# Kernel optimization log

Hardware: AMD Instinct MI355X
Metric: run time of the kernel (lower is better)

## Reference

```python
import jax, jax.numpy as jnp
import numpy as np

E = 2_000_000
N = 50_000   # num nodes / agents (static for segment ops)
D = 32       # emb_dim
L = 2        # num_layers


def setup_inputs() -> dict:
    key = jax.random.key(0)
    ks = jax.random.split(key, 20)
    s = 0.1
    inp = {
        'edge_attr': jax.random.normal(ks[0], (E, 1), jnp.float32),
        'edge_index': jax.random.randint(ks[1], (2, E), 0, N, jnp.int32),
        'w_in': jax.random.normal(ks[2], (1, D)) * s,
        'b_in': jax.random.normal(ks[3], (D,)) * s,
        'tw1': jax.random.normal(ks[4], (L, D, D)) * s,
        'tb1': jax.random.normal(ks[5], (L, D)) * s,
        'tw2': jax.random.normal(ks[6], (L, D, D)) * s,
        'tb2': jax.random.normal(ks[7], (L, D)) * s,
        'uw1': jax.random.normal(ks[8], (L, 2 * D, D)) * s,
        'ub1': jax.random.normal(ks[9], (L, D)) * s,
        'uw2': jax.random.normal(ks[10], (L, D, D)) * s,
        'ub2': jax.random.normal(ks[11], (L, D)) * s,
        'hw1': jax.random.normal(ks[12], (2 * D, D)) * s,
        'hb1': jax.random.normal(ks[13], (D,)) * s,
        'hw2': jax.random.normal(ks[14], (D, D)) * s,
        'hb2': jax.random.normal(ks[15], (D,)) * s,
        'hw3': jax.random.normal(ks[16], (D, 1)) * s,
        'hb3': jax.random.normal(ks[17], (1,)) * s,
    }
    return inp


def reference(edge_attr, edge_index, w_in, b_in, tw1, tb1, tw2, tb2,
              uw1, ub1, uw2, ub2, hw1, hb1, hw2, hb2, hw3, hb3):
    lrelu = jax.nn.leaky_relu  # negative_slope=0.01, matches torch default
    idx = edge_index[0]  # [E] source node per edge

    h0 = edge_attr @ w_in + b_in      # [E, D]
    h = h0
    for l in range(L):
        # per-edge transform MLP
        t = lrelu(h @ tw1[l] + tb1[l]) @ tw2[l] + tb2[l]          # [E, D]
        # scatter_add over source node, then gather back
        s = jax.ops.segment_sum(t, idx, num_segments=N)            # [N, D]
        a = jnp.concatenate([h, s[idx]], axis=-1)                  # [E, 2D]
        h = lrelu(a @ uw1[l] + ub1[l]) @ uw2[l] + ub2[l]           # [E, D]

    hcat = jnp.concatenate([h0, h], axis=-1)                       # [E, 2D]
    v = lrelu(hcat @ hw1 + hb1)
    v = lrelu(v @ hw2 + hb2)
    values = (v @ hw3 + hb3)[:, 0]                                 # [E]

    # constraint == 'sum': scatter_softmax over edge_index[0], times 1.0
    m = jax.ops.segment_max(values, idx, num_segments=N)           # [N]
    e = jnp.exp(values - m[idx])
    d = jax.ops.segment_sum(e, idx, num_segments=N)                # [N]
    votes = (e / d[idx])[:, None] * 1.0                            # [E, 1]
    return votes
```

## Files before the change

### kernel.cpp

```cpp
#include <hip/hip_runtime.h>

#define NN 50000
#define DD 32
#define BLK 256

typedef float f32x4 __attribute__((ext_vector_type(4)));
typedef _Float16 f16x8 __attribute__((ext_vector_type(8)));
typedef __fp16 fp16x2 __attribute__((ext_vector_type(2)));

struct __align__(8) EdgeRec {
    float a;
    int src;
};

union H8 {
    f16x8 h;
    unsigned u[4];
    uint4 u4;
};

__device__ __forceinline__ float lrelu(float x) { return fmaxf(x, 0.01f * x); }

__device__ __forceinline__ f32x4 lrelu4(f32x4 v) {
    f32x4 r;
    r[0] = fmaxf(v[0], 0.01f * v[0]);
    r[1] = fmaxf(v[1], 0.01f * v[1]);
    r[2] = fmaxf(v[2], 0.01f * v[2]);
    r[3] = fmaxf(v[3], 0.01f * v[3]);
    return r;
}

__device__ __forceinline__ unsigned pkrtz(float a, float b) {
    union {
        fp16x2 h;
        unsigned u;
    } x;
    x.h = __builtin_amdgcn_cvt_pkrtz(a, b);
    return x.u;
}

__device__ __forceinline__ f32x4 ld4(const float* __restrict__ p) {
    return *(const f32x4*)p;
}

__device__ __forceinline__ void lds_copy(float* dst, const float* __restrict__ src, int n) {
    for (int i = threadIdx.x; i < n; i += blockDim.x) dst[i] = src[i];
}

__global__ __launch_bounds__(256) void k_hist(const int* __restrict__ ei, int* __restrict__ cnt,
                                              int nE) {
    int e = blockIdx.x * 256 + threadIdx.x;
    if (e < nE) atomicAdd(&cnt[ei[e]], 1);
}

__global__ __launch_bounds__(1024) void k_scan(int* __restrict__ cnt_cur, int* __restrict__ off,
                                               int nN) {
    __shared__ int part[1024];
    int t = threadIdx.x;
    const int CH = (nN + 1023) / 1024;
    int beg = t * CH, end = min(beg + CH, nN);
    int sum = 0;
    for (int i = beg; i < end; ++i) sum += cnt_cur[i];
    part[t] = sum;
    __syncthreads();
    for (int ofs = 1; ofs < 1024; ofs <<= 1) {
        int v = (t >= ofs) ? part[t - ofs] : 0;
        __syncthreads();
        part[t] += v;
        __syncthreads();
    }
    int run = (t == 0) ? 0 : part[t - 1];
    for (int i = beg; i < end; ++i) {
        int c = cnt_cur[i];
        off[i] = run;
        cnt_cur[i] = run;
        run += c;
    }
    if (t == 1023) off[nN] = part[1023];
}

__global__ __launch_bounds__(256) void k_fill(const int* __restrict__ ei,
                                              const float* __restrict__ ea, int* __restrict__ cur,
                                              EdgeRec* __restrict__ rec, int* __restrict__ inv,
                                              int nE) {
    int e = blockIdx.x * 256 + threadIdx.x;
    if (e >= nE) return;
    int src = ei[e];
    int pos = atomicAdd(&cur[src], 1);
    reinterpret_cast<int2*>(rec)[pos] = make_int2(__float_as_int(ea[e]), src);
    inv[e] = pos;
}

__global__ __launch_bounds__(256) void k_bstart(const int* __restrict__ offs,
                                                int* __restrict__ nstart, int nB, int nE) {
    int b = blockIdx.x * 256 + threadIdx.x;
    if (b > nB) return;
    int s = min(b * BLK, nE - 1);
    int lo = 0, hi = NN - 1;
    while (lo < hi) {
        int mid = (lo + hi + 1) >> 1;
        if (offs[mid] <= s) lo = mid;
        else hi = mid - 1;
    }
    nstart[b] = lo;
}

__global__ __launch_bounds__(192) void k_prep(const float* __restrict__ w_in,
                                              const float* __restrict__ b_in,
                                              const float* __restrict__ tw1,
                                              const float* __restrict__ tb1,
                                              const float* __restrict__ uw1,
                                              const float* __restrict__ ub1,
                                              const float* __restrict__ hw1,
                                              const float* __restrict__ hb1,
                                              float* __restrict__ pre) {
    int t = threadIdx.x;
    int which = t >> 5, f = t & 31;
    if (which >= 6) return;
    const float* W = (which < 2) ? tw1 : (which < 4) ? uw1 : hw1;
    const float* x = (which & 1) ? b_in : w_in;
    const float* badd = (which == 1) ? tb1 : (which == 3) ? ub1 : (which == 5) ? hb1 : nullptr;
    float s = badd ? badd[f] : 0.f;
    for (int k = 0; k < 32; ++k) s = fmaf(x[k], W[k * 32 + f], s);
    pre[which * 32 + f] = s;
}

__global__ __launch_bounds__(256) void k_prep2(
    const float* __restrict__ tw1, const float* __restrict__ tb1, const float* __restrict__ tw2,
    const float* __restrict__ tb2, const float* __restrict__ uw1, const float* __restrict__ ub1,
    const float* __restrict__ uw2, const float* __restrict__ ub2, const float* __restrict__ hw1,
    const float* __restrict__ hw2, const float* __restrict__ pre, float* __restrict__ fold,
    unsigned* __restrict__ fragu) {
    for (int e = threadIdx.x; e < 5 * 1024 + 5 * 32; e += 256) {
        if (e < 5120) {
            int m = e >> 10, r = e & 1023, i = r >> 5, j = r & 31;
            const float* A;
            const float* B;
            switch (m) {
                case 0: A = uw2;        B = uw1 + 2048; break;
                case 1: A = uw2;        B = tw1 + 1024; break;
                case 2: A = tw2;        B = uw1 + 1024; break;
                case 3: A = tw2 + 1024; B = uw1 + 3072; break;
                default: A = uw2 + 1024; B = hw1 + 1024; break;
            }
            float s = 0.f;
            for (int k = 0; k < 32; ++k) s = fmaf(A[i * 32 + k], B[k * 32 + j], s);
            fold[e] = s;
        } else {
            int r = e - 5120;
            int v = r >> 5, f = r & 31;
            const float* x;
            const float* B;
            float s;
            switch (v) {
                case 0: x = ub2;      B = tw1 + 1024; s = tb1[32 + f]; break;
                case 1: x = tb2;      B = uw1 + 1024; s = 0.f;         break;
                case 2: x = tb2 + 32; B = uw1 + 3072; s = 0.f;         break;
                case 3: x = ub2;      B = uw1 + 2048; s = ub1[32 + f]; break;
                default: x = ub2 + 32; B = hw1 + 1024; s = pre[160 + f]; break;
            }
            for (int k = 0; k < 32; ++k) s = fmaf(x[k], B[k * 32 + f], s);
            fold[e] = s;
        }
    }
    __syncthreads();
    for (int idx = threadIdx.x; idx < 2048; idx += 256) {
        int d = idx & 3;
        int l = (idx >> 2) & 63;
        int T = (idx >> 8) & 1;
        int m = idx >> 9;
        int row = 16 * T + (l & 15);
        int k0 = ((l >> 4) << 3) + 2 * d;
        const float* W = (m == 0) ? fold + 1024 : (m == 1) ? fold : (m == 2) ? fold + 4096 : hw2;
        int phi = (m == 3) ? row : (((row >> 2) & 3) * 8 + ((row >> 4) << 2) + (row & 3));
        union {
            _Float16 h[2];
            unsigned u;
        } P;
        P.h[0] = (_Float16)W[k0 * 32 + phi];
        P.h[1] = (_Float16)W[(k0 + 1) * 32 + phi];
        fragu[idx] = P.u;
    }
}

__global__ __launch_bounds__(256) void k_accum0f(const EdgeRec* __restrict__ rec,
                                                 const int* __restrict__ offs,
                                                 const int* __restrict__ nstart,
                                                 const float* __restrict__ pre,
                                                 float* __restrict__ M0, int nE) {
    __shared__ float zs[256 * 33];
    __shared__ int woff[260];
    __shared__ int sh2[2];
    int tid = threadIdx.x, b = blockIdx.x;
    int s0 = b * BLK, s1 = min(s0 + BLK, nE);
    if (tid == 0) {
        int nlo = nstart[b];
        sh2[0] = nlo;
        sh2[1] = nstart[b + 1] - nlo + 1;
    }
    __syncthreads();
    int nlo = sh2[0], nwin = sh2[1];
    for (int i = tid; i < nwin + 1; i += 256) woff[i] = offs[nlo + i];
    int s = s0 + tid;
    if (s < s1) {
        float a = rec[s].a;
#pragma unroll
        for (int f = 0; f < DD; ++f) zs[tid * 33 + f] = lrelu(fmaf(a, pre[f], pre[32 + f]));
    }
    __syncthreads();
    for (int t = tid; t < nwin * DD; t += 256) {
        int ln = t >> 5, f = t & 31;
        int lo = max(woff[ln], s0), hi = min(woff[ln + 1], s1);
        if (lo >= hi) continue;
        float sum = 0.f;
        for (int j = lo; j < hi; ++j) sum += zs[(j - s0) * 33 + f];
        int n = nlo + ln;
        bool interior = (woff[ln] >= s0) && (woff[ln + 1] <= s1);
        if (interior) M0[(size_t)n * DD + f] = sum;
        else atomicAdd(&M0[(size_t)n * DD + f], sum);
    }
}

__global__ __launch_bounds__(256) void k_gnode(const float* __restrict__ M,
                                               const float* __restrict__ W,
                                               const float* __restrict__ dv,
                                               const float* __restrict__ addv,
                                               const int* __restrict__ off, float* __restrict__ g) {
    __shared__ float LW[1088];
    lds_copy(LW, W, 1024);
    lds_copy(LW + 1024, dv, 32);
    lds_copy(LW + 1056, addv, 32);
    __syncthreads();
    int tid = blockIdx.x * 256 + threadIdx.x;
    int n = tid >> 5, f = tid & 31;
    if (n >= NN) return;
    float deg = (float)(off[n + 1] - off[n]);
    const float* srow = M + (size_t)n * DD;
    float acc = fmaf(deg, LW[1024 + f], LW[1056 + f]);
    for (int k = 0; k < 32; ++k) acc = fmaf(srow[k], LW[k * 32 + f], acc);
    g[(size_t)n * DD + f] = acc;
}

__global__ __launch_bounds__(256) void k_z1m(const EdgeRec* __restrict__ rec,
                                             const int* __restrict__ offs,
                                             const int* __restrict__ nstart,
                                             const float* __restrict__ pre,
                                             const float* __restrict__ fold,
                                             const unsigned* __restrict__ fragu,
                                             const float* __restrict__ g1, float* __restrict__ Z1,
                                             int nE) {
    __shared__ __align__(16) float zs[256 * 36];
    __shared__ int woff[260];
    __shared__ int sh2[2];
    int tid = threadIdx.x, b = blockIdx.x;
    int s0 = b * BLK, s1 = min(s0 + BLK, nE);
    if (tid == 0) {
        int nlo = nstart[b];
        sh2[0] = nlo;
        sh2[1] = nstart[b + 1] - nlo + 1;
    }
    __syncthreads();
    int nlo = sh2[0], nwin = sh2[1];
    for (int i = tid; i < nwin + 1; i += 256) woff[i] = offs[nlo + i];

    int l = tid & 63, g = l >> 4, e = l & 15, wv = tid >> 6;
    const uint4* fb = (const uint4*)fragu;
    H8 WB0, WB1;
    WB0.u4 = fb[0 + l];
    WB1.u4 = fb[64 + l];
    f32x4 cua = ld4(pre + 64 + 8 * g), cub = ld4(pre + 64 + 8 * g + 4);
    f32x4 vBa = ld4(fold + 5120 + 8 * g), vBb = ld4(fold + 5120 + 8 * g + 4);

    for (int c = 0; c < 4; ++c) {
        int ls = wv * 64 + c * 16 + e;
        int slot = s0 + ls;
        int sc = min(slot, nE - 1);
        EdgeRec r = rec[sc];
        float a = r.a;
        const float* g1p = g1 + (size_t)r.src * DD + 8 * g;
        f32x4 ma = lrelu4(a * cua + ld4(g1p));
        f32x4 mb = lrelu4(a * cub + ld4(g1p + 4));
        H8 B;
        B.u[0] = pkrtz(ma[0], ma[1]);
        B.u[1] = pkrtz(ma[2], ma[3]);
        B.u[2] = pkrtz(mb[0], mb[1]);
        B.u[3] = pkrtz(mb[2], mb[3]);
        f32x4 z0 = __builtin_amdgcn_mfma_f32_16x16x32_f16(WB0.h, B.h, vBa, 0, 0, 0);
        f32x4 z1 = __builtin_amdgcn_mfma_f32_16x16x32_f16(WB1.h, B.h, vBb, 0, 0, 0);
        z0 = lrelu4(z0);
        z1 = lrelu4(z1);
        *(f32x4*)&zs[ls * 36 + 8 * g] = z0;
        *(f32x4*)&zs[ls * 36 + 8 * g + 4] = z1;
    }
    __syncthreads();
    for (int t = tid; t < nwin * DD; t += 256) {
        int ln = t >> 5, f = t & 31;
        int lo = max(woff[ln], s0), hi = min(woff[ln + 1], s1);
        if (lo >= hi) continue;
        float sum = 0.f;
        for (int j = lo; j < hi; ++j) sum += zs[(j - s0) * 36 + f];
        int n = nlo + ln;
        bool interior = (woff[ln] >= s0) && (woff[ln + 1] <= s1);
        if (interior) Z1[(size_t)n * DD + f] = sum;
        else atomicAdd(&Z1[(size_t)n * DD + f], sum);
    }
}

__global__ __launch_bounds__(256) void k_head3m(
    const EdgeRec* __restrict__ rec, const int* __restrict__ offs, const int* __restrict__ nstart,
    const float* __restrict__ pre, const float* __restrict__ fold,
    const unsigned* __restrict__ fragu, const float* __restrict__ hb2,
    const float* __restrict__ hw3, const float* __restrict__ hb3, const float* __restrict__ g1,
    const float* __restrict__ g2, float* __restrict__ ev, float* __restrict__ denom, int nE) {
    __shared__ float evs[256];
    __shared__ int woff[260];
    __shared__ int sh2[2];
    int tid = threadIdx.x, b = blockIdx.x;
    int s0 = b * BLK, s1 = min(s0 + BLK, nE);
    if (tid == 0) {
        int nlo = nstart[b];
        sh2[0] = nlo;
        sh2[1] = nstart[b + 1] - nlo + 1;
    }
    evs[tid] = 0.f;
    __syncthreads();
    int nlo = sh2[0], nwin = sh2[1];
    for (int i = tid; i < nwin + 1; i += 256) woff[i] = offs[nlo + i];

    int l = tid & 63, g = l >> 4, e = l & 15, wv = tid >> 6;
    const uint4* fb = (const uint4*)fragu;
    H8 WA0, WA1, WE0, WE1, H0, H1;
    WA0.u4 = fb[128 + l];
    WA1.u4 = fb[192 + l];
    WE0.u4 = fb[256 + l];
    WE1.u4 = fb[320 + l];
    H0.u4 = fb[384 + l];
    H1.u4 = fb[448 + l];
    f32x4 cua = ld4(pre + 64 + 8 * g), cub = ld4(pre + 64 + 8 * g + 4);
    f32x4 cha = ld4(pre + 128 + 8 * g), chb = ld4(pre + 128 + 8 * g + 4);
    f32x4 dha = ld4(fold + 5248 + 8 * g), dhb = ld4(fold + 5248 + 8 * g + 4);
    f32x4 hb2a = ld4(hb2 + 4 * g), hb2b = ld4(hb2 + 16 + 4 * g);
    f32x4 h3a = ld4(hw3 + 4 * g), h3b = ld4(hw3 + 16 + 4 * g);
    float hb3s = hb3[0];

    for (int c = 0; c < 4; ++c) {
        int ls = wv * 64 + c * 16 + e;
        int slot = s0 + ls;
        int sc = min(slot, nE - 1);
        EdgeRec r = rec[sc];
        float a = r.a;
        const float* g1p = g1 + (size_t)r.src * DD + 8 * g;
        f32x4 ma = lrelu4(a * cua + ld4(g1p));
        f32x4 mb = lrelu4(a * cub + ld4(g1p + 4));
        H8 B;
        B.u[0] = pkrtz(ma[0], ma[1]);
        B.u[1] = pkrtz(ma[2], ma[3]);
        B.u[2] = pkrtz(mb[0], mb[1]);
        B.u[3] = pkrtz(mb[2], mb[3]);
        const float* g2p = g2 + (size_t)r.src * DD + 8 * g;
        f32x4 z0 = ld4(g2p), z1 = ld4(g2p + 4);
        z0 = __builtin_amdgcn_mfma_f32_16x16x32_f16(WA0.h, B.h, z0, 0, 0, 0);
        z1 = __builtin_amdgcn_mfma_f32_16x16x32_f16(WA1.h, B.h, z1, 0, 0, 0);
        z0 = lrelu4(z0);
        z1 = lrelu4(z1);
        B.u[0] = pkrtz(z0[0], z0[1]);
        B.u[1] = pkrtz(z0[2], z0[3]);
        B.u[2] = pkrtz(z1[0], z1[1]);
        B.u[3] = pkrtz(z1[2], z1[3]);
        f32x4 v0 = a * cha + dha, v1 = a * chb + dhb;
        v0 = __builtin_amdgcn_mfma_f32_16x16x32_f16(WE0.h, B.h, v0, 0, 0, 0);
        v1 = __builtin_amdgcn_mfma_f32_16x16x32_f16(WE1.h, B.h, v1, 0, 0, 0);
        v0 = lrelu4(v0);
        v1 = lrelu4(v1);
        B.u[0] = pkrtz(v0[0], v0[1]);
        B.u[1] = pkrtz(v0[2], v0[3]);
        B.u[2] = pkrtz(v1[0], v1[1]);
        B.u[3] = pkrtz(v1[2], v1[3]);
        f32x4 w0 = hb2a, w1 = hb2b;
        w0 = __builtin_amdgcn_mfma_f32_16x16x32_f16(H0.h, B.h, w0, 0, 0, 0);
        w1 = __builtin_amdgcn_mfma_f32_16x16x32_f16(H1.h, B.h, w1, 0, 0, 0);
        w0 = lrelu4(w0);
        w1 = lrelu4(w1);
        f32x4 t = w0 * h3a + w1 * h3b;
        float val = t[0] + t[1] + t[2] + t[3];
        val += __shfl_xor(val, 16, 64);
        val += __shfl_xor(val, 32, 64);
        float exv = __expf(val + hb3s);
        if (g == 0 && slot < s1) {
            ev[slot] = exv;
            evs[ls] = exv;
        }
    }
    __syncthreads();
    for (int t = tid; t < nwin; t += 256) {
        int lo = max(woff[t], s0), hi = min(woff[t + 1], s1);
        if (lo >= hi) continue;
        float sum = 0.f;
        for (int j = lo; j < hi; ++j) sum += evs[j - s0];
        int n = nlo + t;
        bool interior = (woff[t] >= s0) && (woff[t + 1] <= s1);
        if (interior) denom[n] = sum;
        else atomicAdd(&denom[n], sum);
    }
}

__global__ __launch_bounds__(256) void k_final(const int* __restrict__ inv,
                                               const int* __restrict__ ei,
                                               const float* __restrict__ ev,
                                               const float* __restrict__ denom,
                                               float* __restrict__ out, int nE) {
    int e = blockIdx.x * 256 + threadIdx.x;
    if (e >= nE) return;
    out[e] = ev[inv[e]] / denom[ei[e]];
}

extern "C" void kernel_launch(void* const* d_in, const int* in_sizes, int n_in, void* d_out,
                              int out_size, void* d_ws, size_t ws_size, hipStream_t stream) {
    const float* ea = (const float*)d_in[0];
    const int* ei = (const int*)d_in[1];
    const float* w_in = (const float*)d_in[2];
    const float* b_in = (const float*)d_in[3];
    const float* tw1 = (const float*)d_in[4];
    const float* tb1 = (const float*)d_in[5];
    const float* tw2 = (const float*)d_in[6];
    const float* tb2 = (const float*)d_in[7];
    const float* uw1 = (const float*)d_in[8];
    const float* ub1 = (const float*)d_in[9];
    const float* uw2 = (const float*)d_in[10];
    const float* ub2 = (const float*)d_in[11];
    const float* hw1 = (const float*)d_in[12];
    const float* hb1 = (const float*)d_in[13];
    const float* hw2 = (const float*)d_in[14];
    const float* hb2 = (const float*)d_in[15];
    const float* hw3 = (const float*)d_in[16];
    const float* hb3 = (const float*)d_in[17];

    const int nE = in_sizes[0];
    const int gridB = (nE + BLK - 1) / BLK;

    char* w = (char*)d_ws;
    size_t pos = 0;
    auto alloc = [&](size_t bytes) -> void* {
        void* p = w + pos;
        pos = (pos + bytes + 255) & ~(size_t)255;
        return p;
    };
    int* cnt = (int*)alloc((size_t)NN * 4);
    int* offs = (int*)alloc((size_t)(NN + 1) * 4);
    int* nstart = (int*)alloc((size_t)(gridB + 1) * 4);
    EdgeRec* rec = (EdgeRec*)alloc((size_t)nE * sizeof(EdgeRec));
    int* inv = (int*)alloc((size_t)nE * 4);
    float* M0 = (float*)alloc((size_t)NN * DD * 4);
    float* Z1 = (float*)alloc((size_t)NN * DD * 4);
    float* denom = (float*)alloc((size_t)NN * 4);
    float* g1 = (float*)alloc((size_t)NN * DD * 4);
    float* g2 = (float*)alloc((size_t)NN * DD * 4);
    float* ev = (float*)alloc((size_t)nE * 4);
    float* pre = (float*)alloc(6 * 32 * 4);
    float* fold = (float*)alloc((5 * 1024 + 5 * 32) * 4);
    unsigned* fragu = (unsigned*)alloc(2048 * 4);

    hipMemsetAsync(cnt, 0, (size_t)NN * 4, stream);
    hipMemsetAsync(M0, 0, ((size_t)2 * NN * DD + NN) * 4 + 512, stream);

    int gridE = (nE + 255) / 256;
    int gridNF = (NN * DD + 255) / 256;

    k_prep<<<1, 192, 0, stream>>>(w_in, b_in, tw1, tb1, uw1, ub1, hw1, hb1, pre);
    k_prep2<<<1, 256, 0, stream>>>(tw1, tb1, tw2, tb2, uw1, ub1, uw2, ub2, hw1, hw2, pre, fold,
                                   fragu);
    k_hist<<<gridE, 256, 0, stream>>>(ei, cnt, nE);
    k_scan<<<1, 1024, 0, stream>>>(cnt, offs, NN);
    k_fill<<<gridE, 256, 0, stream>>>(ei, ea, cnt, rec, inv, nE);
    k_bstart<<<(gridB + 256) / 256, 256, 0, stream>>>(offs, nstart, gridB, nE);

    k_accum0f<<<gridB, 256, 0, stream>>>(rec, offs, nstart, pre, M0, nE);
    k_gnode<<<gridNF, 256, 0, stream>>>(M0, fold + 2048, fold + 5152, pre + 96, offs, g1);

    k_z1m<<<gridB, 256, 0, stream>>>(rec, offs, nstart, pre, fold, fragu, g1, Z1, nE);
    k_gnode<<<gridNF, 256, 0, stream>>>(Z1, fold + 3072, fold + 5184, fold + 5216, offs, g2);

    k_head3m<<<gridB, 256, 0, stream>>>(rec, offs, nstart, pre, fold, fragu, hb2, hw3, hb3, g1, g2,
                                        ev, denom, nE);
    k_final<<<gridE, 256, 0, stream>>>(inv, ei, ev, denom, (float*)d_out, nE);
}
```

Measured before the change: 674.8 us.

## Two-pass bucketed CSR fill, derive node from window, scatter exp values directly

Replaces the single-pass atomic CSR fill with a coarse bucket pass (128-node buckets) followed by a per-node pass, so the random writes into the sorted edge records are more localized. The record now stores the original edge id instead of the source; kernels recover the node from the block's offset window through a shared-memory lookup. The head kernel writes exp values straight to the output at the original edge position, and the final pass divides in place, which removes the inv and ev arrays. The cost is an extra scan, an extra fill kernel with staging buffers aliased onto M0, a memset moved later, and extra LDS setup and syncs in two kernels.

```diff
diff --git a/kernel.cpp b/kernel.cpp
--- a/kernel.cpp
+++ b/kernel.cpp
@@ -3,6 +3,8 @@
 #define NN 50000
 #define DD 32
 #define BLK 256
+#define BSH 7
+#define NB 512
 
 typedef float f32x4 __attribute__((ext_vector_type(4)));
 typedef _Float16 f16x8 __attribute__((ext_vector_type(8)));
@@ -10,7 +12,7 @@
 
 struct __align__(8) EdgeRec {
     float a;
-    int src;
+    int e;
 };
 
 union H8 {
@@ -47,10 +49,13 @@
     for (int i = threadIdx.x; i < n; i += blockDim.x) dst[i] = src[i];
 }
 
-__global__ __launch_bounds__(256) void k_hist(const int* __restrict__ ei, int* __restrict__ cnt,
-                                              int nE) {
+__global__ __launch_bounds__(256) void k_hist2(const int* __restrict__ ei, int* __restrict__ cnt,
+                                               int* __restrict__ bh, int nE) {
     int e = blockIdx.x * 256 + threadIdx.x;
-    if (e < nE) atomicAdd(&cnt[ei[e]], 1);
+    if (e >= nE) return;
+    int src = ei[e];
+    atomicAdd(&cnt[src], 1);
+    atomicAdd(&bh[src >> BSH], 1);
 }
 
 __global__ __launch_bounds__(1024) void k_scan(int* __restrict__ cnt_cur, int* __restrict__ off,
@@ -79,16 +84,29 @@
     if (t == 1023) off[nN] = part[1023];
 }
 
-__global__ __launch_bounds__(256) void k_fill(const int* __restrict__ ei,
-                                              const float* __restrict__ ea, int* __restrict__ cur,
-                                              EdgeRec* __restrict__ rec, int* __restrict__ inv,
-                                              int nE) {
+__global__ __launch_bounds__(256) void k_fillA(const int* __restrict__ ei,
+                                               const float* __restrict__ ea,
+                                               int* __restrict__ bcur, float* __restrict__ sa,
+                                               int* __restrict__ se, int* __restrict__ ss,
+                                               int nE) {
     int e = blockIdx.x * 256 + threadIdx.x;
     if (e >= nE) return;
     int src = ei[e];
-    int pos = atomicAdd(&cur[src], 1);
-    reinterpret_cast<int2*>(rec)[pos] = make_int2(__float_as_int(ea[e]), src);
-    inv[e] = pos;
+    int pos = atomicAdd(&bcur[src >> BSH], 1);
+    sa[pos] = ea[e];
+    se[pos] = e;
+    ss[pos] = src;
+}
+
+__global__ __launch_bounds__(256) void k_fillB(const float* __restrict__ sa,
+                                               const int* __restrict__ se,
+                                               const int* __restrict__ ss, int* __restrict__ cur,
+                                               EdgeRec* __restrict__ rec, int nE) {
+    int p = blockIdx.x * 256 + threadIdx.x;
+    if (p >= nE) return;
+    int src = ss[p];
+    int slot = atomicAdd(&cur[src], 1);
+    reinterpret_cast<int2*>(rec)[slot] = make_int2(__float_as_int(sa[p]), se[p]);
 }
 
 __global__ __launch_bounds__(256) void k_bstart(const int* __restrict__ offs,
@@ -251,6 +269,7 @@
                                              int nE) {
     __shared__ __align__(16) float zs[256 * 36];
     __shared__ int woff[260];
+    __shared__ int snode[BLK];
     __shared__ int sh2[2];
     int tid = threadIdx.x, b = blockIdx.x;
     int s0 = b * BLK, s1 = min(s0 + BLK, nE);
@@ -259,9 +278,16 @@
         sh2[0] = nlo;
         sh2[1] = nstart[b + 1] - nlo + 1;
     }
+    snode[tid] = 0;
     __syncthreads();
     int nlo = sh2[0], nwin = sh2[1];
     for (int i = tid; i < nwin + 1; i += 256) woff[i] = offs[nlo + i];
+    __syncthreads();
+    for (int t = tid; t < nwin; t += 256) {
+        int lo = max(woff[t], s0), hi = min(woff[t + 1], s1);
+        for (int j = lo; j < hi; ++j) snode[j - s0] = t;
+    }
+    __syncthreads();
 
     int l = tid & 63, g = l >> 4, e = l & 15, wv = tid >> 6;
     const uint4* fb = (const uint4*)fragu;
@@ -275,9 +301,9 @@
         int ls = wv * 64 + c * 16 + e;
         int slot = s0 + ls;
         int sc = min(slot, nE - 1);
-        EdgeRec r = rec[sc];
-        float a = r.a;
-        const float* g1p = g1 + (size_t)r.src * DD + 8 * g;
+        float a = rec[sc].a;
+        int n = nlo + snode[ls];
+        const float* g1p = g1 + (size_t)n * DD + 8 * g;
         f32x4 ma = lrelu4(a * cua + ld4(g1p));
         f32x4 mb = lrelu4(a * cub + ld4(g1p + 4));
         H8 B;
@@ -311,9 +337,10 @@
     const float* __restrict__ pre, const float* __restrict__ fold,
     const unsigned* __restrict__ fragu, const float* __restrict__ hb2,
     const float* __restrict__ hw3, const float* __restrict__ hb3, const float* __restrict__ g1,
-    const float* __restrict__ g2, float* __restrict__ ev, float* __restrict__ denom, int nE) {
+    const float* __restrict__ g2, float* __restrict__ out, float* __restrict__ denom, int nE) {
     __shared__ float evs[256];
     __shared__ int woff[260];
+    __shared__ int snode[BLK];
     __shared__ int sh2[2];
     int tid = threadIdx.x, b = blockIdx.x;
     int s0 = b * BLK, s1 = min(s0 + BLK, nE);
@@ -323,9 +350,16 @@
         sh2[1] = nstart[b + 1] - nlo + 1;
     }
     evs[tid] = 0.f;
+    snode[tid] = 0;
     __syncthreads();
     int nlo = sh2[0], nwin = sh2[1];
     for (int i = tid; i < nwin + 1; i += 256) woff[i] = offs[nlo + i];
+    __syncthreads();
+    for (int t = tid; t < nwin; t += 256) {
+        int lo = max(woff[t], s0), hi = min(woff[t + 1], s1);
+        for (int j = lo; j < hi; ++j) snode[j - s0] = t;
+    }
+    __syncthreads();
 
     int l = tid & 63, g = l >> 4, e = l & 15, wv = tid >> 6;
     const uint4* fb = (const uint4*)fragu;
@@ -349,7 +383,8 @@
         int sc = min(slot, nE - 1);
         EdgeRec r = rec[sc];
         float a = r.a;
-        const float* g1p = g1 + (size_t)r.src * DD + 8 * g;
+        int n = nlo + snode[ls];
+        const float* g1p = g1 + (size_t)n * DD + 8 * g;
         f32x4 ma = lrelu4(a * cua + ld4(g1p));
         f32x4 mb = lrelu4(a * cub + ld4(g1p + 4));
         H8 B;
@@ -357,7 +392,7 @@
         B.u[1] = pkrtz(ma[2], ma[3]);
         B.u[2] = pkrtz(mb[0], mb[1]);
         B.u[3] = pkrtz(mb[2], mb[3]);
-        const float* g2p = g2 + (size_t)r.src * DD + 8 * g;
+        const float* g2p = g2 + (size_t)n * DD + 8 * g;
         f32x4 z0 = ld4(g2p), z1 = ld4(g2p + 4);
         z0 = __builtin_amdgcn_mfma_f32_16x16x32_f16(WA0.h, B.h, z0, 0, 0, 0);
         z1 = __builtin_amdgcn_mfma_f32_16x16x32_f16(WA1.h, B.h, z1, 0, 0, 0);
@@ -387,7 +422,7 @@
         val += __shfl_xor(val, 32, 64);
         float exv = __expf(val + hb3s);
         if (g == 0 && slot < s1) {
-            ev[slot] = exv;
+            out[r.e] = exv;
             evs[ls] = exv;
         }
     }
@@ -404,14 +439,12 @@
     }
 }
 
-__global__ __launch_bounds__(256) void k_final(const int* __restrict__ inv,
-                                               const int* __restrict__ ei,
-                                               const float* __restrict__ ev,
-                                               const float* __restrict__ denom,
-                                               float* __restrict__ out, int nE) {
+__global__ __launch_bounds__(256) void k_div(const int* __restrict__ ei,
+                                             const float* __restrict__ denom,
+                                             float* __restrict__ out, int nE) {
     int e = blockIdx.x * 256 + threadIdx.x;
     if (e >= nE) return;
-    out[e] = ev[inv[e]] / denom[ei[e]];
+    out[e] = out[e] / denom[ei[e]];
 }
 
 extern "C" void kernel_launch(void* const* d_in, const int* in_sizes, int n_in, void* d_out,
@@ -446,22 +479,25 @@
         return p;
     };
     int* cnt = (int*)alloc((size_t)NN * 4);
+    int* bh = (int*)alloc((size_t)NB * 4);
     int* offs = (int*)alloc((size_t)(NN + 1) * 4);
+    int* boff = (int*)alloc((size_t)(NB + 1) * 4);
     int* nstart = (int*)alloc((size_t)(gridB + 1) * 4);
     EdgeRec* rec = (EdgeRec*)alloc((size_t)nE * sizeof(EdgeRec));
-    int* inv = (int*)alloc((size_t)nE * 4);
     float* M0 = (float*)alloc((size_t)NN * DD * 4);
     float* Z1 = (float*)alloc((size_t)NN * DD * 4);
     float* denom = (float*)alloc((size_t)NN * 4);
     float* g1 = (float*)alloc((size_t)NN * DD * 4);
     float* g2 = (float*)alloc((size_t)NN * DD * 4);
-    float* ev = (float*)alloc((size_t)nE * 4);
     float* pre = (float*)alloc(6 * 32 * 4);
     float* fold = (float*)alloc((5 * 1024 + 5 * 32) * 4);
     unsigned* fragu = (unsigned*)alloc(2048 * 4);
 
-    hipMemsetAsync(cnt, 0, (size_t)NN * 4, stream);
-    hipMemsetAsync(M0, 0, ((size_t)2 * NN * DD + NN) * 4 + 512, stream);
+    float* sa = M0;
+    int* se = (int*)M0 + (size_t)nE;
+    int* ss = (int*)M0 + (size_t)2 * nE;
+
+    hipMemsetAsync(cnt, 0, (size_t)((char*)offs - (char*)cnt), stream);
 
     int gridE = (nE + 255) / 256;
     int gridNF = (NN * DD + 255) / 256;
@@ -469,10 +505,14 @@
     k_prep<<<1, 192, 0, stream>>>(w_in, b_in, tw1, tb1, uw1, ub1, hw1, hb1, pre);
     k_prep2<<<1, 256, 0, stream>>>(tw1, tb1, tw2, tb2, uw1, ub1, uw2, ub2, hw1, hw2, pre, fold,
                                    fragu);
-    k_hist<<<gridE, 256, 0, stream>>>(ei, cnt, nE);
+    k_hist2<<<gridE, 256, 0, stream>>>(ei, cnt, bh, nE);
     k_scan<<<1, 1024, 0, stream>>>(cnt, offs, NN);
-    k_fill<<<gridE, 256, 0, stream>>>(ei, ea, cnt, rec, inv, nE);
+    k_scan<<<1, 1024, 0, stream>>>(bh, boff, NB);
+    k_fillA<<<gridE, 256, 0, stream>>>(ei, ea, bh, sa, se, ss, nE);
+    k_fillB<<<gridE, 256, 0, stream>>>(sa, se, ss, cnt, rec, nE);
     k_bstart<<<(gridB + 256) / 256, 256, 0, stream>>>(offs, nstart, gridB, nE);
+
+    hipMemsetAsync(M0, 0, (size_t)((char*)g1 - (char*)M0), stream);
 
     k_accum0f<<<gridB, 256, 0, stream>>>(rec, offs, nstart, pre, M0, nE);
     k_gnode<<<gridNF, 256, 0, stream>>>(M0, fold + 2048, fold + 5152, pre + 96, offs, g1);
@@ -481,6 +521,6 @@
     k_gnode<<<gridNF, 256, 0, stream>>>(Z1, fold + 3072, fold + 5184, fold + 5216, offs, g2);
 
     k_head3m<<<gridB, 256, 0, stream>>>(rec, offs, nstart, pre, fold, fragu, hb2, hw3, hb3, g1, g2,
-                                        ev, denom, nE);
-    k_final<<<gridE, 256, 0, stream>>>(inv, ei, ev, denom, (float*)d_out, nE);
-}
+                                        (float*)d_out, denom, nE);
+    k_div<<<gridE, 256, 0, stream>>>(ei, denom, (float*)d_out, nE);
+}
```

Measured after the change: 1.944 ms. 188% more time.
